# Optimization experiments

Measured on AMD Instinct MI355X. Metric: run time of the kernel, lower is better.

## Reference

```python
import jax, jax.numpy as jnp
import numpy as np

B, S, IN, H, OUT = 512, 1024, 32, 128, 1


def setup_inputs() -> dict:
    key = jax.random.key(0)
    ks = jax.random.split(key, 7)
    sc = 1.0 / np.sqrt(H)  # torch LSTM/Linear default init scale
    return {
        "x": jax.random.normal(ks[0], (B, S, IN), dtype=jnp.float32),
        "W_ih": jax.random.normal(ks[1], (4 * H, IN), dtype=jnp.float32) * sc,
        "W_hh": jax.random.normal(ks[2], (4 * H, H), dtype=jnp.float32) * sc,
        "b_ih": jax.random.normal(ks[3], (4 * H,), dtype=jnp.float32) * sc,
        "b_hh": jax.random.normal(ks[4], (4 * H,), dtype=jnp.float32) * sc,
        "W_lin": jax.random.normal(ks[5], (OUT, H * S), dtype=jnp.float32) * (1.0 / np.sqrt(H * S)),
        "b_lin": jax.random.normal(ks[6], (OUT,), dtype=jnp.float32) * (1.0 / np.sqrt(H * S)),
    }


def _lstm(x, W_ih, W_hh, b_ih, b_hh):
    # x: [B,S,IN]. Precompute input projection for all timesteps (one big GEMM).
    xw = jnp.einsum("bsi,gi->bsg", x, W_ih) + (b_ih + b_hh)  # [B,S,4H]
    h0 = jnp.zeros((x.shape[0], W_hh.shape[1]), dtype=x.dtype)
    c0 = jnp.zeros_like(h0)

    def step(carry, xw_t):
        h, c = carry
        gates = xw_t + h @ W_hh.T  # [B,4H]
        i, f, g, o = jnp.split(gates, 4, axis=-1)  # torch gate order i,f,g,o
        i = jax.nn.sigmoid(i)
        f = jax.nn.sigmoid(f)
        g = jnp.tanh(g)
        o = jax.nn.sigmoid(o)
        c = f * c + i * g
        h = o * jnp.tanh(c)
        return (h, c), h

    (_, _), hs = jax.lax.scan(step, (h0, c0), jnp.swapaxes(xw, 0, 1))  # hs: [S,B,H]
    return jnp.swapaxes(hs, 0, 1)  # [B,S,H]


def reference(x, W_ih, W_hh, b_ih, b_hh, W_lin, b_lin):
    lstm_out = _lstm(x, W_ih, W_hh, b_ih, b_hh)          # [B,S,H]
    flat = lstm_out.reshape(lstm_out.shape[0], -1)        # [B,S*H]
    return flat @ W_lin.T + b_lin                         # [B,OUT]
```

## Files before the change

### kernel.cpp

```cpp
#include <hip/hip_runtime.h>
#include <stdint.h>

constexpr int B = 512, S = 1024, IN = 32, H = 128;
constexpr int KTOT = IN + H;
constexpr int KSL = KTOT / 4;
constexpr int KP = KSL / 2;

typedef uint32_t u32;

template <int CTRL>
__device__ __forceinline__ float dpp_qp(float v) {
  return __int_as_float(__builtin_amdgcn_update_dpp(
      0, __float_as_int(v), CTRL, 0xF, 0xF, true));
}
__device__ __forceinline__ void dot2(float& c, u32 a, u32 b) {
  asm("v_dot2_f32_f16 %0, %1, %2, %0" : "+v"(c) : "v"(a), "v"(b));
}
__device__ __forceinline__ float sigm(float v) {
  float e = __builtin_amdgcn_exp2f(-1.4426950408889634f * v);
  return __builtin_amdgcn_rcpf(1.0f + e);
}
__device__ __forceinline__ float tanh_(float v) {
  float e = __builtin_amdgcn_exp2f(-2.8853900817779268f * v);
  return 2.0f * __builtin_amdgcn_rcpf(1.0f + e) - 1.0f;
}

__global__ __launch_bounds__(512, 2)
void lstm_fused(const float* __restrict__ x, const float* __restrict__ Wih,
                const float* __restrict__ Whh, const float* __restrict__ bih,
                const float* __restrict__ bhh, const float* __restrict__ Wlin,
                const float* __restrict__ blin, float* __restrict__ out) {
  __shared__ alignas(16) _Float16 hx[2][2][KTOT];
  __shared__ float red[2 * H];

  const int tid = threadIdx.x;
  const int g = tid >> 2;
  const int j = tid & 3;
  const int b0 = blockIdx.x * 2;

  u32 w[4][KP];
#pragma unroll
  for (int c = 0; c < 4; ++c) {
    const int n = c * H + g;
#pragma unroll
    for (int p = 0; p < KP; ++p) {
      const int k0 = KSL * j + 2 * p;
      const int k1 = k0 + 1;
      const float f0 = (k0 < IN) ? Wih[n * IN + k0] : Whh[n * H + (k0 - IN)];
      const float f1 = (k1 < IN) ? Wih[n * IN + k1] : Whh[n * H + (k1 - IN)];
      union { _Float16 h[2]; u32 u; } cv;
      cv.h[0] = (_Float16)f0;
      cv.h[1] = (_Float16)f1;
      w[c][p] = cv.u;
    }
  }
#pragma unroll
  for (int c = 0; c < 4; ++c)
#pragma unroll
    for (int p = 0; p < KP; ++p) asm volatile("" : "+v"(w[c][p]));

  float bias[4];
#pragma unroll
  for (int c = 0; c < 4; ++c) bias[c] = bih[c * H + g] + bhh[c * H + g];

  if (tid < 2 * KTOT) ((_Float16*)hx)[tid] = (_Float16)0.0f;
  __syncthreads();
  if (tid < 2 * IN) {
    const int b = tid >> 5, k = tid & 31;
    hx[0][b][k] = (_Float16)x[(size_t)(b0 + b) * (S * IN) + k];
  }
  __syncthreads();

  float cc = 0.f;
  float oa = 0.f;
  const int xb = g >> 5, xk = g & 31;
  const int bb = j & 1;

  for (int s = 0; s < S; ++s) {
    const int p = s & 1, np = p ^ 1;
    float wl = 0.f, xn = 0.f;
    if (j < 2) wl = Wlin[s * H + g];
    const bool xload = (j == 2) && (g < 64) && (s + 1 < S);
    if (xload) xn = x[(size_t)(b0 + xb) * (S * IN) + (s + 1) * IN + xk];

    float acc[4][2];
#pragma unroll
    for (int c = 0; c < 4; ++c) { acc[c][0] = 0.f; acc[c][1] = 0.f; }
#pragma unroll
    for (int b = 0; b < 2; ++b) {
      const uint4* pp = reinterpret_cast<const uint4*>(&hx[p][b][KSL * j]);
#pragma unroll
      for (int q = 0; q < 5; ++q) {
        const uint4 v = pp[q];
        const u32 e[4] = {v.x, v.y, v.z, v.w};
#pragma unroll
        for (int u = 0; u < 4; ++u)
#pragma unroll
          for (int c = 0; c < 4; ++c) dot2(acc[c][b], e[u], w[c][4 * q + u]);
      }
    }
#pragma unroll
    for (int c = 0; c < 4; ++c)
#pragma unroll
      for (int b = 0; b < 2; ++b) {
        float v = acc[c][b];
        v += dpp_qp<0xB1>(v);
        v += dpp_qp<0x4E>(v);
        acc[c][b] = v;
      }
    const float gi = sigm(acc[0][bb] + bias[0]);
    const float gf = sigm(acc[1][bb] + bias[1]);
    const float gg = tanh_(acc[2][bb] + bias[2]);
    const float go = sigm(acc[3][bb] + bias[3]);
    cc = gf * cc + gi * gg;
    const float h = go * tanh_(cc);
    if (j < 2) {
      hx[np][bb][IN + g] = (_Float16)h;
      oa += h * wl;
    } else if (xload) {
      hx[np][xb][xk] = (_Float16)xn;
    }
    __syncthreads();
  }

  if (j < 2) red[j * H + g] = oa;
  __syncthreads();
  if (tid < 2) {
    float sum = blin[0];
    for (int k = 0; k < H; ++k) sum += red[tid * H + k];
    out[b0 + tid] = sum;
  }
}

extern "C" void kernel_launch(void* const* d_in, const int* in_sizes, int n_in,
                              void* d_out, int out_size, void* d_ws, size_t ws_size,
                              hipStream_t stream) {
  const float* x    = (const float*)d_in[0];
  const float* Wih  = (const float*)d_in[1];
  const float* Whh  = (const float*)d_in[2];
  const float* bih  = (const float*)d_in[3];
  const float* bhh  = (const float*)d_in[4];
  const float* Wlin = (const float*)d_in[5];
  const float* blin = (const float*)d_in[6];
  float* outp = (float*)d_out;
  hipLaunchKernelGGL(lstm_fused, dim3(B / 2), dim3(512), 0, stream,
                     x, Wih, Whh, bih, bhh, Wlin, blin, outp);
}
```

Baseline: 1.473 ms.

## Process one batch row per block with LDS cross-wave gate reduction

Each block now handles a single batch element instead of two, so the grid doubles to 512 blocks and launch bounds request four blocks per CU. The K-slice partial sums move from intra-quad DPP shuffles to a shared-memory reduction across waves. Two designated waves, chosen by block parity, apply the gate nonlinearities. This halves the per-step dot work per block and spreads the batch across more blocks for more concurrency. In exchange it adds an extra __syncthreads per timestep and LDS round trips, and every block keeps its own register-resident copy of the weights.

Result: faster. 1.264 ms (-14.2%).

```diff
diff --git a/kernel.cpp b/kernel.cpp
--- a/kernel.cpp
+++ b/kernel.cpp
@@ -3,16 +3,12 @@
 
 constexpr int B = 512, S = 1024, IN = 32, H = 128;
 constexpr int KTOT = IN + H;
-constexpr int KSL = KTOT / 4;
+constexpr int NJ = 4;
+constexpr int KSL = KTOT / NJ;
 constexpr int KP = KSL / 2;
 
 typedef uint32_t u32;
 
-template <int CTRL>
-__device__ __forceinline__ float dpp_qp(float v) {
-  return __int_as_float(__builtin_amdgcn_update_dpp(
-      0, __float_as_int(v), CTRL, 0xF, 0xF, true));
-}
 __device__ __forceinline__ void dot2(float& c, u32 a, u32 b) {
   asm("v_dot2_f32_f16 %0, %1, %2, %0" : "+v"(c) : "v"(a), "v"(b));
 }
@@ -25,110 +21,109 @@
   return 2.0f * __builtin_amdgcn_rcpf(1.0f + e) - 1.0f;
 }
 
-__global__ __launch_bounds__(512, 2)
+__global__ __launch_bounds__(512, 4)
 void lstm_fused(const float* __restrict__ x, const float* __restrict__ Wih,
                 const float* __restrict__ Whh, const float* __restrict__ bih,
                 const float* __restrict__ bhh, const float* __restrict__ Wlin,
                 const float* __restrict__ blin, float* __restrict__ out) {
-  __shared__ alignas(16) _Float16 hx[2][2][KTOT];
-  __shared__ float red[2 * H];
+  __shared__ alignas(16) _Float16 hx[2][KTOT];
+  __shared__ alignas(16) float red[NJ][H][4];
+  __shared__ float redf[H];
 
   const int tid = threadIdx.x;
-  const int g = tid >> 2;
-  const int j = tid & 3;
-  const int b0 = blockIdx.x * 2;
+  const int lane = tid & 63;
+  const int w = tid >> 6;
+  const int j = w >> 1;
+  const int g = (w & 1) * 64 + lane;
+  const int b = blockIdx.x;
+  const int par = b & 1;
+  const int aw0 = par, aw1 = 6 + par;
+  const bool isact = (w == aw0) || (w == aw1);
+  const int ga = (w == aw0) ? lane : 64 + lane;
+  const int xw = 2 + par;
 
-  u32 w[4][KP];
+  u32 wreg[4][KP];
 #pragma unroll
   for (int c = 0; c < 4; ++c) {
     const int n = c * H + g;
 #pragma unroll
-    for (int p = 0; p < KP; ++p) {
-      const int k0 = KSL * j + 2 * p;
-      const int k1 = k0 + 1;
+    for (int pq = 0; pq < KP; ++pq) {
+      const int k0 = KSL * j + 2 * pq, k1 = k0 + 1;
       const float f0 = (k0 < IN) ? Wih[n * IN + k0] : Whh[n * H + (k0 - IN)];
       const float f1 = (k1 < IN) ? Wih[n * IN + k1] : Whh[n * H + (k1 - IN)];
       union { _Float16 h[2]; u32 u; } cv;
       cv.h[0] = (_Float16)f0;
       cv.h[1] = (_Float16)f1;
-      w[c][p] = cv.u;
+      wreg[c][pq] = cv.u;
     }
   }
 #pragma unroll
   for (int c = 0; c < 4; ++c)
 #pragma unroll
-    for (int p = 0; p < KP; ++p) asm volatile("" : "+v"(w[c][p]));
+    for (int pq = 0; pq < KP; ++pq) asm volatile("" : "+v"(wreg[c][pq]));
 
-  float bias[4];
+  float bias_a[4] = {0.f, 0.f, 0.f, 0.f};
+  if (isact) {
 #pragma unroll
-  for (int c = 0; c < 4; ++c) bias[c] = bih[c * H + g] + bhh[c * H + g];
+    for (int c = 0; c < 4; ++c) bias_a[c] = bih[c * H + ga] + bhh[c * H + ga];
+  }
 
-  if (tid < 2 * KTOT) ((_Float16*)hx)[tid] = (_Float16)0.0f;
-  __syncthreads();
-  if (tid < 2 * IN) {
-    const int b = tid >> 5, k = tid & 31;
-    hx[0][b][k] = (_Float16)x[(size_t)(b0 + b) * (S * IN) + k];
+  const size_t xbase = (size_t)b * S * IN;
+  if (tid < KTOT) {
+    hx[0][tid] = (tid < IN) ? (_Float16)x[xbase + tid] : (_Float16)0.0f;
+    hx[1][tid] = (_Float16)0.0f;
   }
   __syncthreads();
 
-  float cc = 0.f;
-  float oa = 0.f;
-  const int xb = g >> 5, xk = g & 31;
-  const int bb = j & 1;
+  float cc = 0.f, oa = 0.f;
 
   for (int s = 0; s < S; ++s) {
     const int p = s & 1, np = p ^ 1;
     float wl = 0.f, xn = 0.f;
-    if (j < 2) wl = Wlin[s * H + g];
-    const bool xload = (j == 2) && (g < 64) && (s + 1 < S);
-    if (xload) xn = x[(size_t)(b0 + xb) * (S * IN) + (s + 1) * IN + xk];
+    if (isact) wl = Wlin[s * H + ga];
+    const bool xload = (w == xw) && (lane < IN) && (s + 1 < S);
+    if (xload) xn = x[xbase + (s + 1) * IN + lane];
 
-    float acc[4][2];
+    const uint4* pp =
+        (const uint4*)((const char*)&hx[p][0] + j * (KSL * 2));
+    float acc[4] = {0.f, 0.f, 0.f, 0.f};
 #pragma unroll
-    for (int c = 0; c < 4; ++c) { acc[c][0] = 0.f; acc[c][1] = 0.f; }
+    for (int q = 0; q < 5; ++q) {
+      const uint4 v = pp[q];
+      const u32 e[4] = {v.x, v.y, v.z, v.w};
 #pragma unroll
-    for (int b = 0; b < 2; ++b) {
-      const uint4* pp = reinterpret_cast<const uint4*>(&hx[p][b][KSL * j]);
+      for (int u = 0; u < 4; ++u)
 #pragma unroll
-      for (int q = 0; q < 5; ++q) {
-        const uint4 v = pp[q];
-        const u32 e[4] = {v.x, v.y, v.z, v.w};
-#pragma unroll
-        for (int u = 0; u < 4; ++u)
-#pragma unroll
-          for (int c = 0; c < 4; ++c) dot2(acc[c][b], e[u], w[c][4 * q + u]);
-      }
+        for (int c = 0; c < 4; ++c) dot2(acc[c], e[u], wreg[c][4 * q + u]);
     }
-#pragma unroll
-    for (int c = 0; c < 4; ++c)
-#pragma unroll
-      for (int b = 0; b < 2; ++b) {
-        float v = acc[c][b];
-        v += dpp_qp<0xB1>(v);
-        v += dpp_qp<0x4E>(v);
-        acc[c][b] = v;
-      }
-    const float gi = sigm(acc[0][bb] + bias[0]);
-    const float gf = sigm(acc[1][bb] + bias[1]);
-    const float gg = tanh_(acc[2][bb] + bias[2]);
-    const float go = sigm(acc[3][bb] + bias[3]);
-    cc = gf * cc + gi * gg;
-    const float h = go * tanh_(cc);
-    if (j < 2) {
-      hx[np][bb][IN + g] = (_Float16)h;
+    *(float4*)&red[j][g][0] = make_float4(acc[0], acc[1], acc[2], acc[3]);
+    __syncthreads();
+
+    if (isact) {
+      const float4 r0 = *(const float4*)&red[0][ga][0];
+      const float4 r1 = *(const float4*)&red[1][ga][0];
+      const float4 r2 = *(const float4*)&red[2][ga][0];
+      const float4 r3 = *(const float4*)&red[3][ga][0];
+      const float gi = sigm(r0.x + r1.x + r2.x + r3.x + bias_a[0]);
+      const float gf = sigm(r0.y + r1.y + r2.y + r3.y + bias_a[1]);
+      const float gg = tanh_(r0.z + r1.z + r2.z + r3.z + bias_a[2]);
+      const float go = sigm(r0.w + r1.w + r2.w + r3.w + bias_a[3]);
+      cc = gf * cc + gi * gg;
+      const float h = go * tanh_(cc);
+      hx[np][IN + ga] = (_Float16)h;
       oa += h * wl;
     } else if (xload) {
-      hx[np][xb][xk] = (_Float16)xn;
+      hx[np][lane] = (_Float16)xn;
     }
     __syncthreads();
   }
 
-  if (j < 2) red[j * H + g] = oa;
+  if (isact) redf[ga] = oa;
   __syncthreads();
-  if (tid < 2) {
+  if (tid == 0) {
     float sum = blin[0];
-    for (int k = 0; k < H; ++k) sum += red[tid * H + k];
-    out[b0 + tid] = sum;
+    for (int k = 0; k < H; ++k) sum += redf[k];
+    out[b] = sum;
   }
 }
 
@@ -143,6 +138,6 @@
   const float* Wlin = (const float*)d_in[5];
   const float* blin = (const float*)d_in[6];
   float* outp = (float*)d_out;
-  hipLaunchKernelGGL(lstm_fused, dim3(B / 2), dim3(512), 0, stream,
+  hipLaunchKernelGGL(lstm_fused, dim3(B), dim3(512), 0, stream,
                      x, Wih, Whh, bih, bhh, Wlin, blin, outp);
 }
```

## Stage x and W_lin in 32-step LDS chunks and split K per lane

Applied to the files above, without the earlier changes.

Every 32 timesteps the kernel loads x and W_lin in bulk with float4 reads into double-buffered shared memory, replacing the per-step scalar global loads that sat on the recurrent critical path. The K split is reorganized so each lane handles 8 input and 32 hidden weights, reading x and h from separate LDS arrays. All four lanes now compute both batch rows' gates redundantly so the dpp-reduced results are used directly. Launch bounds drop to one block per SM-equivalent, and the redundant transcendental math adds some ALU work per step.

New measurement: 1.343 ms. 1.1x faster.

```diff
diff --git a/kernel.cpp b/kernel.cpp
--- a/kernel.cpp
+++ b/kernel.cpp
@@ -2,9 +2,7 @@
 #include <stdint.h>
 
 constexpr int B = 512, S = 1024, IN = 32, H = 128;
-constexpr int KTOT = IN + H;
-constexpr int KSL = KTOT / 4;
-constexpr int KP = KSL / 2;
+constexpr int CH = 32;
 
 typedef uint32_t u32;
 
@@ -24,111 +22,154 @@
   float e = __builtin_amdgcn_exp2f(-2.8853900817779268f * v);
   return 2.0f * __builtin_amdgcn_rcpf(1.0f + e) - 1.0f;
 }
+__device__ __forceinline__ u32 pack2(float a, float b) {
+  union { _Float16 h[2]; u32 u; } cv;
+  cv.h[0] = (_Float16)a;
+  cv.h[1] = (_Float16)b;
+  return cv.u;
+}
 
-__global__ __launch_bounds__(512, 2)
+__global__ __launch_bounds__(512, 1)
 void lstm_fused(const float* __restrict__ x, const float* __restrict__ Wih,
                 const float* __restrict__ Whh, const float* __restrict__ bih,
                 const float* __restrict__ bhh, const float* __restrict__ Wlin,
                 const float* __restrict__ blin, float* __restrict__ out) {
-  __shared__ alignas(16) _Float16 hx[2][2][KTOT];
-  __shared__ float red[2 * H];
+  __shared__ alignas(16) _Float16 hxh[2][2][H];
+  __shared__ alignas(16) u32 xc[2][CH][2][IN / 2];
+  __shared__ alignas(16) float wc[2][CH * H];
+  __shared__ float redf[2][H];
 
   const int tid = threadIdx.x;
   const int g = tid >> 2;
   const int j = tid & 3;
-  const int b0 = blockIdx.x * 2;
+  const int r0 = blockIdx.x * 2;
+  const size_t xb0 = (size_t)r0 * S * IN, xb1 = xb0 + (size_t)S * IN;
 
-  u32 w[4][KP];
+  u32 wr[4][20];
 #pragma unroll
   for (int c = 0; c < 4; ++c) {
     const int n = c * H + g;
 #pragma unroll
-    for (int p = 0; p < KP; ++p) {
-      const int k0 = KSL * j + 2 * p;
-      const int k1 = k0 + 1;
-      const float f0 = (k0 < IN) ? Wih[n * IN + k0] : Whh[n * H + (k0 - IN)];
-      const float f1 = (k1 < IN) ? Wih[n * IN + k1] : Whh[n * H + (k1 - IN)];
-      union { _Float16 h[2]; u32 u; } cv;
-      cv.h[0] = (_Float16)f0;
-      cv.h[1] = (_Float16)f1;
-      w[c][p] = cv.u;
-    }
+    for (int u = 0; u < 4; ++u)
+      wr[c][u] = pack2(Wih[n * IN + 8 * j + 2 * u],
+                       Wih[n * IN + 8 * j + 2 * u + 1]);
+#pragma unroll
+    for (int e = 0; e < 16; ++e)
+      wr[c][4 + e] = pack2(Whh[n * H + 32 * j + 2 * e],
+                           Whh[n * H + 32 * j + 2 * e + 1]);
   }
 #pragma unroll
   for (int c = 0; c < 4; ++c)
 #pragma unroll
-    for (int p = 0; p < KP; ++p) asm volatile("" : "+v"(w[c][p]));
+    for (int e = 0; e < 20; ++e) asm volatile("" : "+v"(wr[c][e]));
 
   float bias[4];
 #pragma unroll
   for (int c = 0; c < 4; ++c) bias[c] = bih[c * H + g] + bhh[c * H + g];
 
-  if (tid < 2 * KTOT) ((_Float16*)hx)[tid] = (_Float16)0.0f;
-  __syncthreads();
-  if (tid < 2 * IN) {
-    const int b = tid >> 5, k = tid & 31;
-    hx[0][b][k] = (_Float16)x[(size_t)(b0 + b) * (S * IN) + k];
+  if (tid < 2 * 2 * H / 2) ((u32*)hxh)[tid] = 0u;
+
+  const int rw = tid >> 8, rem = tid & 255, so = rem >> 3, k4 = (rem & 7) * 4;
+  {
+    const float4 xv = *(const float4*)&x[(rw ? xb1 : xb0) + so * IN + k4];
+    const float4 wv0 = *(const float4*)&Wlin[tid * 8];
+    const float4 wv1 = *(const float4*)&Wlin[tid * 8 + 4];
+    *(uint2*)&xc[0][so][rw][k4 >> 1] =
+        make_uint2(pack2(xv.x, xv.y), pack2(xv.z, xv.w));
+    *(float4*)&wc[0][tid * 8] = wv0;
+    *(float4*)&wc[0][tid * 8 + 4] = wv1;
   }
   __syncthreads();
 
-  float cc = 0.f;
-  float oa = 0.f;
-  const int xb = g >> 5, xk = g & 31;
-  const int bb = j & 1;
+  float cc0 = 0.f, cc1 = 0.f, oa0 = 0.f, oa1 = 0.f;
+  float4 pxv = make_float4(0, 0, 0, 0);
+  float4 pwv0 = pxv, pwv1 = pxv;
 
   for (int s = 0; s < S; ++s) {
-    const int p = s & 1, np = p ^ 1;
-    float wl = 0.f, xn = 0.f;
-    if (j < 2) wl = Wlin[s * H + g];
-    const bool xload = (j == 2) && (g < 64) && (s + 1 < S);
-    if (xload) xn = x[(size_t)(b0 + xb) * (S * IN) + (s + 1) * IN + xk];
+    const int t = s & (CH - 1), cb = (s >> 5) & 1, p = s & 1, np = p ^ 1;
 
-    float acc[4][2];
+    if (t == 0 && s + CH < S) {
+      pxv = *(const float4*)&x[(rw ? xb1 : xb0) + (size_t)(s + CH + so) * IN + k4];
+      pwv0 = *(const float4*)&Wlin[(size_t)(s + CH) * H + tid * 8];
+      pwv1 = *(const float4*)&Wlin[(size_t)(s + CH) * H + tid * 8 + 4];
+    }
+    if (t == 1 && s - 1 + CH < S) {
+      *(uint2*)&xc[cb ^ 1][so][rw][k4 >> 1] =
+          make_uint2(pack2(pxv.x, pxv.y), pack2(pxv.z, pxv.w));
+      *(float4*)&wc[cb ^ 1][tid * 8] = pwv0;
+      *(float4*)&wc[cb ^ 1][tid * 8 + 4] = pwv1;
+    }
+
+    float a00 = 0.f, a10 = 0.f, a20 = 0.f, a30 = 0.f;
+    float a01 = 0.f, a11 = 0.f, a21 = 0.f, a31 = 0.f;
+    {
+      const uint4 xq0 = *(const uint4*)&xc[cb][t][0][j * 4];
+      const uint4 xq1 = *(const uint4*)&xc[cb][t][1][j * 4];
+      const u32 e0[4] = {xq0.x, xq0.y, xq0.z, xq0.w};
+      const u32 e1[4] = {xq1.x, xq1.y, xq1.z, xq1.w};
 #pragma unroll
-    for (int c = 0; c < 4; ++c) { acc[c][0] = 0.f; acc[c][1] = 0.f; }
+      for (int u = 0; u < 4; ++u) {
+        dot2(a00, e0[u], wr[0][u]); dot2(a01, e1[u], wr[0][u]);
+        dot2(a10, e0[u], wr[1][u]); dot2(a11, e1[u], wr[1][u]);
+        dot2(a20, e0[u], wr[2][u]); dot2(a21, e1[u], wr[2][u]);
+        dot2(a30, e0[u], wr[3][u]); dot2(a31, e1[u], wr[3][u]);
+      }
+      const uint4* h0 = (const uint4*)&hxh[p][0][0];
+      const uint4* h1 = (const uint4*)&hxh[p][1][0];
 #pragma unroll
-    for (int b = 0; b < 2; ++b) {
-      const uint4* pp = reinterpret_cast<const uint4*>(&hx[p][b][KSL * j]);
+      for (int q = 0; q < 4; ++q) {
+        const uint4 hv0 = h0[4 * j + q];
+        const uint4 hv1 = h1[4 * j + q];
+        const u32 f0[4] = {hv0.x, hv0.y, hv0.z, hv0.w};
+        const u32 f1[4] = {hv1.x, hv1.y, hv1.z, hv1.w};
 #pragma unroll
-      for (int q = 0; q < 5; ++q) {
-        const uint4 v = pp[q];
-        const u32 e[4] = {v.x, v.y, v.z, v.w};
-#pragma unroll
-        for (int u = 0; u < 4; ++u)
-#pragma unroll
-          for (int c = 0; c < 4; ++c) dot2(acc[c][b], e[u], w[c][4 * q + u]);
+        for (int u = 0; u < 4; ++u) {
+          dot2(a00, f0[u], wr[0][4 + 4 * q + u]);
+          dot2(a01, f1[u], wr[0][4 + 4 * q + u]);
+          dot2(a10, f0[u], wr[1][4 + 4 * q + u]);
+          dot2(a11, f1[u], wr[1][4 + 4 * q + u]);
+          dot2(a20, f0[u], wr[2][4 + 4 * q + u]);
+          dot2(a21, f1[u], wr[2][4 + 4 * q + u]);
+          dot2(a30, f0[u], wr[3][4 + 4 * q + u]);
+          dot2(a31, f1[u], wr[3][4 + 4 * q + u]);
+        }
       }
     }
-#pragma unroll
-    for (int c = 0; c < 4; ++c)
-#pragma unroll
-      for (int b = 0; b < 2; ++b) {
-        float v = acc[c][b];
-        v += dpp_qp<0xB1>(v);
-        v += dpp_qp<0x4E>(v);
-        acc[c][b] = v;
-      }
-    const float gi = sigm(acc[0][bb] + bias[0]);
-    const float gf = sigm(acc[1][bb] + bias[1]);
-    const float gg = tanh_(acc[2][bb] + bias[2]);
-    const float go = sigm(acc[3][bb] + bias[3]);
-    cc = gf * cc + gi * gg;
-    const float h = go * tanh_(cc);
-    if (j < 2) {
-      hx[np][bb][IN + g] = (_Float16)h;
-      oa += h * wl;
-    } else if (xload) {
-      hx[np][xb][xk] = (_Float16)xn;
+#define QRED(v) { float t_ = (v); t_ += dpp_qp<0xB1>(t_); t_ += dpp_qp<0x4E>(t_); (v) = t_; }
+    QRED(a00) QRED(a10) QRED(a20) QRED(a30)
+    QRED(a01) QRED(a11) QRED(a21) QRED(a31)
+#undef QRED
+
+    const float wl = wc[cb][t * H + g];
+    {
+      const float gi = sigm(a00 + bias[0]);
+      const float gf = sigm(a10 + bias[1]);
+      const float gg = tanh_(a20 + bias[2]);
+      const float go = sigm(a30 + bias[3]);
+      cc0 = gf * cc0 + gi * gg;
+      const float h = go * tanh_(cc0);
+      if (j == 0) hxh[np][0][g] = (_Float16)h;
+      oa0 += h * wl;
+    }
+    {
+      const float gi = sigm(a01 + bias[0]);
+      const float gf = sigm(a11 + bias[1]);
+      const float gg = tanh_(a21 + bias[2]);
+      const float go = sigm(a31 + bias[3]);
+      cc1 = gf * cc1 + gi * gg;
+      const float h = go * tanh_(cc1);
+      if (j == 1) hxh[np][1][g] = (_Float16)h;
+      oa1 += h * wl;
     }
     __syncthreads();
   }
 
-  if (j < 2) red[j * H + g] = oa;
+  if (j == 0) { redf[0][g] = oa0; redf[1][g] = oa1; }
   __syncthreads();
   if (tid < 2) {
     float sum = blin[0];
-    for (int k = 0; k < H; ++k) sum += red[tid * H + k];
-    out[b0 + tid] = sum;
+    for (int k = 0; k < H; ++k) sum += redf[tid][k];
+    out[r0 + tid] = sum;
   }
 }
 
```
